# Kernel tuning notes

Hardware: AMD Instinct MI355X
Metric: run time of the kernel (lower is better)

## Reference

```python
import jax, jax.numpy as jnp
import numpy as np

N_NODES = 100000
N_EDGES = 1600000
N_GRAPHS = 64
VOCAB = 50000
D = 128
EPS = 1e-5


def setup_inputs() -> dict:
    key = jax.random.key(0)
    ks = jax.random.split(key, 24)
    tokens = jax.random.randint(ks[0], (N_NODES,), 0, VOCAB)
    src = jax.random.randint(ks[1], (N_EDGES,), 0, N_NODES)
    dst = jax.random.randint(ks[2], (N_EDGES,), 0, N_NODES)
    graph_ids = jnp.sort(jax.random.randint(ks[3], (N_NODES,), 0, N_GRAPHS))
    s = 1.0 / np.sqrt(D)
    inp = {
        'tokens': tokens, 'src': src, 'dst': dst, 'graph_ids': graph_ids,
        'embed': jax.random.normal(ks[4], (VOCAB, D), jnp.float32),
        'W1': jax.random.normal(ks[5], (D, D), jnp.float32) * s,
        'b1': jnp.zeros((D,), jnp.float32),
        'g1': jnp.ones((D,), jnp.float32), 'be1': jnp.zeros((D,), jnp.float32),
        'W2': jax.random.normal(ks[6], (D, D), jnp.float32) * s,
        'b2': jnp.zeros((D,), jnp.float32),
        'g2': jnp.ones((D,), jnp.float32), 'be2': jnp.zeros((D,), jnp.float32),
        'W3': jax.random.normal(ks[7], (D, D), jnp.float32) * s,
        'b3': jnp.zeros((D,), jnp.float32),
        'g3': jnp.ones((D,), jnp.float32), 'be3': jnp.zeros((D,), jnp.float32),
        'fcW1': jax.random.normal(ks[8], (D, D // 2), jnp.float32) * s,
        'fcb1': jnp.zeros((D // 2,), jnp.float32),
        'fcW2': jax.random.normal(ks[9], (D // 2, 2), jnp.float32) * (1.0 / np.sqrt(D // 2)),
        'fcb2': jnp.zeros((2,), jnp.float32),
    }
    return inp


def _graph_conv(h, src, dst, norm_src, norm_dst, W, b):
    # DGL GraphConv, norm='both': D_out^{-1/2} -> sum-aggregate -> D_in^{-1/2} -> linear
    msg = (h * norm_src[:, None])[src]                      # [E, D]
    agg = jax.ops.segment_sum(msg, dst, num_segments=N_NODES)
    return (agg * norm_dst[:, None]) @ W + b


def _bn_relu(h, gamma, beta):
    mu = jnp.mean(h, axis=0)
    var = jnp.mean((h - mu) ** 2, axis=0)                   # biased var (torch BN)
    return jax.nn.relu((h - mu) * jax.lax.rsqrt(var + EPS) * gamma + beta)


def reference(tokens, src, dst, graph_ids, embed,
              W1, b1, g1, be1, W2, b2, g2, be2, W3, b3, g3, be3,
              fcW1, fcb1, fcW2, fcb2):
    ones_e = jnp.ones((N_EDGES,), jnp.float32)
    deg_out = jnp.maximum(jax.ops.segment_sum(ones_e, src, num_segments=N_NODES), 1.0)
    deg_in = jnp.maximum(jax.ops.segment_sum(ones_e, dst, num_segments=N_NODES), 1.0)
    norm_src = jax.lax.rsqrt(deg_out)
    norm_dst = jax.lax.rsqrt(deg_in)

    h = embed[tokens]                                        # [N, D]
    h = _bn_relu(_graph_conv(h, src, dst, norm_src, norm_dst, W1, b1), g1, be1)
    h = _bn_relu(_graph_conv(h, src, dst, norm_src, norm_dst, W2, b2), g2, be2)
    h = _bn_relu(_graph_conv(h, src, dst, norm_src, norm_dst, W3, b3), g3, be3)

    # dgl.mean_nodes per graph
    sums = jax.ops.segment_sum(h, graph_ids, num_segments=N_GRAPHS)  # [G, D]
    cnts = jnp.maximum(jax.ops.segment_sum(jnp.ones((N_NODES,), jnp.float32), graph_ids, num_segments=N_GRAPHS), 1.0)
    hg = sums / cnts[:, None]

    hg = jax.nn.relu(hg @ fcW1 + fcb1)                       # dropout = identity (eval)
    return hg @ fcW2 + fcb2                                  # [G, 2]
```

## Files before the change

kernel.cpp:

```cpp
#include <hip/hip_runtime.h>

#define N_NODES 100000
#define N_EDGES 1600000
#define N_GRAPHS 64
#define DIM 128
#define BN_EPS 1e-5f
#define EPAD 2000000

#define NB_SENT 977
#define NB_WPREP 192
#define NB_HIST 391
#define NB_ZERO 40
#define NBUCK 782
#define NG (NBUCK * NB_HIST)
#define NB_SCANG2 2389
#define BUCK_RESERVE 388

#define AT_STRIDE 136

typedef unsigned short ushort_t;
typedef unsigned char uchar_t;
typedef unsigned int uint_t;
typedef __attribute__((ext_vector_type(8))) short bf16x8;
typedef __attribute__((ext_vector_type(4))) float f32x4;

__device__ __forceinline__ float bfl(uint_t u) {
    union { uint_t i; float f; } v; v.i = u << 16; return v.f;
}
__device__ __forceinline__ float bfh(uint_t u) {
    union { uint_t i; float f; } v; v.i = u & 0xffff0000u; return v.f;
}
__device__ __forceinline__ ushort_t f2bf(float f) {
    union { float f; uint_t i; } v; v.f = f;
    uint_t x = v.i;
    return (ushort_t)((x + 0x7fffu + ((x >> 16) & 1u)) >> 16);
}
__device__ __forceinline__ uint_t pack2(float lo, float hi) {
    return ((uint_t)f2bf(hi) << 16) | (uint_t)f2bf(lo);
}

__global__ void k_front(const int* __restrict__ src, const int* __restrict__ dst,
                        ushort_t* __restrict__ bufA, int* __restrict__ esrc,
                        const float* __restrict__ w1, const float* __restrict__ w2,
                        const float* __restrict__ w3, ushort_t* __restrict__ wbt,
                        int* __restrict__ GG, int* __restrict__ zp, int zwords) {
    __shared__ int hh[NBUCK];
    __shared__ int hh2[NBUCK];
    int b = blockIdx.x;
    int t = threadIdx.x;
    if (b < NB_SENT) {
        int i0 = (b * 256 + t) * 8;
        int4 sv = make_int4(N_NODES, N_NODES, N_NODES, N_NODES);
        if (i0 + 8 <= EPAD) {
            *(int4*)(esrc + i0) = sv;
            *(int4*)(esrc + i0 + 4) = sv;
        } else {
            for (int i = i0; i < EPAD; ++i) esrc[i] = N_NODES;
        }
        if (b == 0 && t < 64)
            ((uint_t*)(bufA + (size_t)N_NODES * DIM))[t] = 0u;
        return;
    }
    b -= NB_SENT;
    if (b < NB_WPREP) {
        int i = b * 256 + t;
        int l = i >> 14;
        int idx = i & (DIM * DIM - 1);
        int n = idx >> 7, k = idx & (DIM - 1);
        const float* wsrc = (l == 0) ? w1 : (l == 1) ? w2 : w3;
        wbt[i] = f2bf(wsrc[k * DIM + n]);
        return;
    }
    b -= NB_WPREP;
    if (b < NB_HIST) {
        for (int k = t; k < NBUCK; k += 256) { hh[k] = 0; hh2[k] = 0; }
        __syncthreads();
        int e0 = b * 4096;
        int e1 = min(e0 + 4096, N_EDGES);
        for (int i = e0 + t; i < e1; i += 256) {
            atomicAdd(&hh[dst[i] >> 7], 1);
            atomicAdd(&hh2[src[i] >> 7], 1);
        }
        __syncthreads();
        for (int k = t; k < NBUCK; k += 256) {
            GG[k * NB_HIST + b] = hh[k];
            GG[NG + k * NB_HIST + b] = hh2[k];
        }
        return;
    }
    b -= NB_HIST;
    {
        int i = b * 256 + t;
        if (i < zwords) zp[i] = 0;
    }
}

__global__ void k_scanA(const int* __restrict__ GG, int* __restrict__ Gs,
                        int* __restrict__ partials) {
    __shared__ int s[256];
    int t = threadIdx.x;
    int i = blockIdx.x * 256 + t;
    int v = (i < 2 * NG) ? GG[i] : 0;
    s[t] = v;
    __syncthreads();
    for (int off = 1; off < 256; off <<= 1) {
        int add = (t >= off) ? s[t - off] : 0;
        __syncthreads();
        s[t] += add;
        __syncthreads();
    }
    if (i < 2 * NG) Gs[i + 1] = s[t];
    if (t == 255) partials[blockIdx.x] = s[t];
}

__global__ void k_scanB(const int* __restrict__ partials, int* __restrict__ Gs) {
    __shared__ int s[256];
    int t = threadIdx.x;
    int p = 0;
    for (int j = t; j < (int)blockIdx.x; j += 256) p += partials[j];
    s[t] = p;
    __syncthreads();
    for (int off = 128; off > 0; off >>= 1) {
        if (t < off) s[t] += s[t + off];
        __syncthreads();
    }
    int prefix = s[0];
    int i = blockIdx.x * 256 + t;
    if (i < 2 * NG) Gs[i + 1] += prefix;
    if (blockIdx.x == 0 && t == 0) Gs[0] = 0;
}

__global__ void k_pass2(const int* __restrict__ src, const int* __restrict__ dst,
                        const int* __restrict__ Gs, uint_t* __restrict__ Cpk,
                        uchar_t* __restrict__ Cls) {
    __shared__ int cur[NBUCK];
    __shared__ int cur2[NBUCK];
    int b = blockIdx.x;
    int t = threadIdx.x;
    for (int k = t; k < NBUCK; k += 256) {
        cur[k] = Gs[k * NB_HIST + b];
        cur2[k] = Gs[NG + k * NB_HIST + b] - N_EDGES;
    }
    __syncthreads();
    int e0 = b * 4096;
    int e1 = min(e0 + 4096, N_EDGES);
    for (int i = e0 + t; i < e1; i += 256) {
        int d = dst[i];
        int s = src[i];
        int slot = atomicAdd(&cur[d >> 7], 1);
        Cpk[slot] = (uint_t)s | ((uint_t)(d & 127) << 17);
        int slot2 = atomicAdd(&cur2[s >> 7], 1);
        Cls[slot2] = (uchar_t)(s & 127);
    }
}

__global__ void k_fine(const uint_t* __restrict__ Cpk, const uchar_t* __restrict__ Cls,
                       const int* __restrict__ Gs,
                       const int* __restrict__ tokens, const float* __restrict__ embed,
                       int* __restrict__ esrc, int* __restrict__ rowptr,
                       int* __restrict__ pdeg, float* __restrict__ ns,
                       float* __restrict__ nd, ushort_t* __restrict__ bufA) {
    __shared__ int hcnt[128];
    __shared__ int hstart[128];
    __shared__ float lns[128];
    int b = blockIdx.x;
    int t = threadIdx.x;
    if (b < NBUCK) {
        int k = b;
        int node0 = k * 128;
        int nn = min(128, N_NODES - node0);
        int S = Gs[k * NB_HIST];
        int E = Gs[(k + 1) * NB_HIST];
        if (t < 128) hcnt[t] = 0;
        __syncthreads();
        for (int i = S + t; i < E; i += 256) atomicAdd(&hcnt[Cpk[i] >> 17], 1);
        __syncthreads();
        if (t == 0) {
            int acc = 0;
            for (int n = 0; n < nn; ++n) {
                hstart[n] = acc;
                acc += (hcnt[n] + 3) & ~3;
            }
        }
        __syncthreads();
        int base = (k * BUCK_RESERVE + S + 3) & ~3;
        if (t < nn) {
            int node = node0 + t;
            rowptr[node] = base + hstart[t];
            pdeg[node] = (hcnt[t] + 3) & ~3;
            nd[node] = rsqrtf(fmaxf((float)hcnt[t], 1.0f));
        }
        __syncthreads();
        for (int i = S + t; i < E; i += 256) {
            uint_t pk = Cpk[i];
            int slot = atomicAdd(&hstart[pk >> 17], 1);
            esrc[base + slot] = (int)(pk & 0x1FFFFu);
        }
    } else {
        int k = b - NBUCK;
        int node0 = k * 128;
        int nn = min(128, N_NODES - node0);
        int S = Gs[NG + k * NB_HIST] - N_EDGES;
        int E = Gs[NG + (k + 1) * NB_HIST] - N_EDGES;
        if (t < 128) hcnt[t] = 0;
        __syncthreads();
        for (int i = S + t; i < E; i += 256) atomicAdd(&hcnt[Cls[i]], 1);
        __syncthreads();
        if (t < nn) {
            float v = rsqrtf(fmaxf((float)hcnt[t], 1.0f));
            ns[node0 + t] = v;
            lns[t] = v;
        }
        if (k == 0 && t == 0) ns[N_NODES] = 0.f;
        __syncthreads();
        for (int slot = t; slot < nn * 16; slot += 256) {
            int nloc = slot >> 4, sub = slot & 15;
            int node = node0 + nloc;
            float s = lns[nloc];
            const float* ep = embed + (size_t)tokens[node] * DIM + sub * 8;
            float4 a = *(const float4*)ep;
            float4 c = *(const float4*)(ep + 4);
            uint4 o;
            o.x = pack2(a.x * s, a.y * s);
            o.y = pack2(a.z * s, a.w * s);
            o.z = pack2(c.x * s, c.y * s);
            o.w = pack2(c.z * s, c.w * s);
            *(uint4*)(bufA + (size_t)node * DIM + sub * 8) = o;
        }
    }
}

__global__ void k_prescale(const ushort_t* __restrict__ yin, const float* __restrict__ ns,
                           const float* __restrict__ bnsum, const float* __restrict__ bnsq,
                           const float* __restrict__ g, const float* __restrict__ be,
                           ushort_t* __restrict__ xout) {
    __shared__ float sa[DIM], sc[DIM];
    int t = threadIdx.x;
    if (t < DIM) {
        float mu = bnsum[t] * (1.0f / N_NODES);
        float var = bnsq[t] * (1.0f / N_NODES) - mu * mu;
        float rstd = rsqrtf(var + BN_EPS);
        float a = g[t] * rstd;
        sa[t] = a;
        sc[t] = be[t] - mu * a;
    }
    __syncthreads();
    int gid = blockIdx.x * 256 + t;
    int node = gid >> 4, sub = gid & 15;
    float s = ns[node];
    uint4 u = *(const uint4*)(yin + (size_t)node * DIM + sub * 8);
    float v[8] = {bfl(u.x), bfh(u.x), bfl(u.y), bfh(u.y),
                  bfl(u.z), bfh(u.z), bfl(u.w), bfh(u.w)};
    const float* a = sa + sub * 8;
    const float* c = sc + sub * 8;
#pragma unroll
    for (int i = 0; i < 8; ++i) v[i] = fmaxf(fmaf(v[i], a[i], c[i]), 0.f) * s;
    uint4 o;
    o.x = pack2(v[0], v[1]); o.y = pack2(v[2], v[3]);
    o.z = pack2(v[4], v[5]); o.w = pack2(v[6], v[7]);
    *(uint4*)(xout + (size_t)node * DIM + sub * 8) = o;
}

__global__ __launch_bounds__(256, 5) void k_agggemm(const ushort_t* __restrict__ hs,
        const int* __restrict__ rowptr, const int* __restrict__ pdeg,
        const int* __restrict__ esrc, const float* __restrict__ nd,
        const ushort_t* __restrict__ wbt, const float* __restrict__ bias,
        ushort_t* __restrict__ y,
        float* __restrict__ bnsum, float* __restrict__ bnsq) {
    __shared__ ushort_t at[64 * AT_STRIDE];
    __shared__ float csum[DIM], csq[DIM];
    int tid = threadIdx.x;
    int wave = tid >> 6;
    int lane = tid & 63;
    if (tid < DIM) { csum[tid] = 0.f; csq[tid] = 0.f; }
    __syncthreads();

    int bnode = blockIdx.x * 64 + wave * 16;
    int quad = lane >> 4;
    int m16 = lane & 15;

    const ushort_t* hrow = hs + (size_t)m16 * 8;

    int rpv = 0, pdv = 0;
    if (lane < 16) {
        int nnode = bnode + lane;
        if (nnode < N_NODES) { rpv = rowptr[nnode]; pdv = pdeg[nnode]; }
    }

#define FEATLD(ix) (*(const uint4*)(hrow + (size_t)(ix) * DIM))
#define ACCU(F, A)                                                  \
    {                                                               \
        A[0] += bfl((F).x); A[1] += bfh((F).x);                     \
        A[2] += bfl((F).y); A[3] += bfh((F).y);                     \
        A[4] += bfl((F).z); A[5] += bfh((F).z);                     \
        A[6] += bfl((F).w); A[7] += bfh((F).w);                     \
    }
#define DRAIN(E, T, A)                                              \
    {                                                               \
        if ((T) >= 2) {                                             \
            int i0_ = esrc[E], i1_ = esrc[(E) + 4];                 \
            (E) += 8; (T) -= 2;                                     \
            uint4 f0_ = FEATLD(i0_), f1_ = FEATLD(i1_);             \
            while ((T) >= 2) {                                      \
                int j0_ = esrc[E], j1_ = esrc[(E) + 4];             \
                (E) += 8; (T) -= 2;                                 \
                ACCU(f0_, A); ACCU(f1_, A);                         \
                f0_ = FEATLD(j0_); f1_ = FEATLD(j1_);               \
            }                                                       \
            ACCU(f0_, A); ACCU(f1_, A);                             \
        }                                                           \
        if (T) {                                                    \
            int i0_ = esrc[E];                                      \
            uint4 f0_ = FEATLD(i0_);                                \
            ACCU(f0_, A);                                           \
        }                                                           \
    }

    for (int i = 0; i < 16; i += 2) {
        int nodeA = bnode + i;
        int nodeB = bnode + i + 1;
        int eA = __shfl(rpv, i) + quad;
        int tA = __shfl(pdv, i) >> 2;
        int eB = __shfl(rpv, i + 1) + quad;
        int tB = __shfl(pdv, i + 1) >> 2;
        float aA[8] = {0.f, 0.f, 0.f, 0.f, 0.f, 0.f, 0.f, 0.f};
        float aB[8] = {0.f, 0.f, 0.f, 0.f, 0.f, 0.f, 0.f, 0.f};
        if (tA >= 2 && tB >= 2) {
            int iA0 = esrc[eA], iA1 = esrc[eA + 4];
            int iB0 = esrc[eB], iB1 = esrc[eB + 4];
            eA += 8; eB += 8; tA -= 2; tB -= 2;
            uint4 fA0 = FEATLD(iA0), fA1 = FEATLD(iA1);
            uint4 fB0 = FEATLD(iB0), fB1 = FEATLD(iB1);
            while (tA >= 2 && tB >= 2) {
                int jA0 = esrc[eA], jA1 = esrc[eA + 4];
                int jB0 = esrc[eB], jB1 = esrc[eB + 4];
                eA += 8; eB += 8; tA -= 2; tB -= 2;
                ACCU(fA0, aA); ACCU(fA1, aA);
                ACCU(fB0, aB); ACCU(fB1, aB);
                fA0 = FEATLD(jA0); fA1 = FEATLD(jA1);
                fB0 = FEATLD(jB0); fB1 = FEATLD(jB1);
            }
            ACCU(fA0, aA); ACCU(fA1, aA);
            ACCU(fB0, aB); ACCU(fB1, aB);
        }
        DRAIN(eA, tA, aA);
        DRAIN(eB, tB, aB);
#pragma unroll
        for (int j = 0; j < 8; ++j) {
            aA[j] += __shfl_xor(aA[j], 16);
            aA[j] += __shfl_xor(aA[j], 32);
            aB[j] += __shfl_xor(aB[j], 16);
            aB[j] += __shfl_xor(aB[j], 32);
        }
        float nA = (nodeA < N_NODES) ? nd[nodeA] : 0.f;
        float nB = (nodeB < N_NODES) ? nd[nodeB] : 0.f;
        if (quad == 0) {
            uint4 oA, oB;
            oA.x = pack2(aA[0] * nA, aA[1] * nA);
            oA.y = pack2(aA[2] * nA, aA[3] * nA);
            oA.z = pack2(aA[4] * nA, aA[5] * nA);
            oA.w = pack2(aA[6] * nA, aA[7] * nA);
            oB.x = pack2(aB[0] * nB, aB[1] * nB);
            oB.y = pack2(aB[2] * nB, aB[3] * nB);
            oB.z = pack2(aB[4] * nB, aB[5] * nB);
            oB.w = pack2(aB[6] * nB, aB[7] * nB);
            *(uint4*)&at[(wave * 16 + i) * AT_STRIDE + m16 * 8] = oA;
            *(uint4*)&at[(wave * 16 + i + 1) * AT_STRIDE + m16 * 8] = oB;
        }
    }
#undef DRAIN
#undef ACCU
#undef FEATLD

    f32x4 acc[8];
#pragma unroll
    for (int nb = 0; nb < 8; ++nb) acc[nb] = (f32x4)(0.f);

    const ushort_t* ap = &at[(wave * 16 + m16) * AT_STRIDE + quad * 8];
#pragma unroll
    for (int k0b = 0; k0b < 4; ++k0b) {
        bf16x8 af = *(const bf16x8*)(ap + k0b * 32);
#pragma unroll
        for (int nb = 0; nb < 8; ++nb) {
            int ncol = nb * 16 + m16;
            bf16x8 bfg = *(const bf16x8*)(wbt + (size_t)ncol * DIM + k0b * 32 + quad * 8);
            acc[nb] = __builtin_amdgcn_mfma_f32_16x16x32_bf16(af, bfg, acc[nb], 0, 0, 0);
        }
    }

#pragma unroll
    for (int nb = 0; nb < 8; ++nb) {
        int col = nb * 16 + m16;
        float bcol = bias[col];
        float ps = 0.f, pq = 0.f;
#pragma unroll
        for (int reg = 0; reg < 4; ++reg) {
            int r = bnode + quad * 4 + reg;
            if (r < N_NODES) {
                float v = acc[nb][reg] + bcol;
                ps += v; pq += v * v;
                y[(size_t)r * DIM + col] = f2bf(v);
            }
        }
        atomicAdd(&csum[col], ps);
        atomicAdd(&csq[col], pq);
    }
    __syncthreads();
    if (tid < DIM) {
        atomicAdd(&bnsum[tid], csum[tid]);
        atomicAdd(&bnsq[tid], csq[tid]);
    }
}

#define POOL_NODES 128
__global__ void k_pool(const ushort_t* __restrict__ yin, const int* __restrict__ gids,
                       const float* __restrict__ bnsum, const float* __restrict__ bnsq,
                       const float* __restrict__ g, const float* __restrict__ be,
                       float* __restrict__ pool, int* __restrict__ cnt) {
    __shared__ int h[N_GRAPHS];
    int col = threadIdx.x;
    float mu = bnsum[col] * (1.0f / N_NODES);
    float var = bnsq[col] * (1.0f / N_NODES) - mu * mu;
    float rstd = rsqrtf(var + BN_EPS);
    float a = g[col] * rstd;
    float c = be[col] - mu * a;
    if (col < N_GRAPHS) h[col] = 0;
    __syncthreads();
    int base = blockIdx.x * POOL_NODES;
    int end = min(base + POOL_NODES, N_NODES);
    for (int n = base + col; n < end; n += 128) atomicAdd(&h[gids[n]], 1);
    __syncthreads();
    if (col < N_GRAPHS && h[col]) atomicAdd(&cnt[col], h[col]);
    float acc = 0.f;
    int cur = gids[base];
    for (int n = base; n < end; ++n) {
        int gg = gids[n];
        if (gg != cur) {
            atomicAdd(&pool[(size_t)cur * DIM + col], acc);
            acc = 0.f;
            cur = gg;
        }
        uint_t u = *(const uint_t*)(yin + (size_t)n * DIM + (col & ~1));
        float v = (col & 1) ? bfh(u) : bfl(u);
        acc += fmaxf(fmaf(v, a, c), 0.f);
    }
    atomicAdd(&pool[(size_t)cur * DIM + col], acc);
}

__global__ void k_final(const float* __restrict__ pool, const int* __restrict__ cnt,
                        const float* __restrict__ fcW1, const float* __restrict__ fcb1,
                        const float* __restrict__ fcW2, const float* __restrict__ fcb2,
                        float* __restrict__ out) {
    __shared__ float hg[DIM];
    __shared__ float z[64];
    int g = blockIdx.x;
    int t = threadIdx.x;
    float cf = fmaxf((float)cnt[g], 1.0f);
    hg[t] = pool[(size_t)g * DIM + t] / cf;
    __syncthreads();
    if (t < 64) {
        float acc = fcb1[t];
        for (int k = 0; k < DIM; ++k)
            acc += hg[k] * fcW1[k * 64 + t];
        z[t] = fmaxf(acc, 0.f);
    }
    __syncthreads();
    if (t < 2) {
        float acc = fcb2[t];
        for (int k = 0; k < 64; ++k)
            acc += z[k] * fcW2[k * 2 + t];
        out[g * 2 + t] = acc;
    }
}

extern "C" void kernel_launch(void* const* d_in, const int* in_sizes, int n_in,
                              void* d_out, int out_size, void* d_ws, size_t ws_size,
                              hipStream_t stream) {
    const int* tokens = (const int*)d_in[0];
    const int* src = (const int*)d_in[1];
    const int* dst = (const int*)d_in[2];
    const int* gids = (const int*)d_in[3];
    const float* embed = (const float*)d_in[4];
    const float* W1 = (const float*)d_in[5];
    const float* b1 = (const float*)d_in[6];
    const float* g1 = (const float*)d_in[7];
    const float* be1 = (const float*)d_in[8];
    const float* W2 = (const float*)d_in[9];
    const float* b2 = (const float*)d_in[10];
    const float* g2 = (const float*)d_in[11];
    const float* be2 = (const float*)d_in[12];
    const float* W3 = (const float*)d_in[13];
    const float* b3 = (const float*)d_in[14];
    const float* g3 = (const float*)d_in[15];
    const float* be3 = (const float*)d_in[16];
    const float* fcW1 = (const float*)d_in[17];
    const float* fcb1 = (const float*)d_in[18];
    const float* fcW2 = (const float*)d_in[19];
    const float* fcb2 = (const float*)d_in[20];
    float* out = (float*)d_out;

    char* w = (char*)d_ws;
    auto alloc = [&](size_t bytes) {
        void* p = (void*)w;
        w += (bytes + 255) & ~(size_t)255;
        return p;
    };
    ushort_t* bufH = (ushort_t*)alloc((size_t)(N_NODES + 1) * DIM * 2);
    ushort_t* bufA = (ushort_t*)alloc((size_t)(N_NODES + 1) * DIM * 2);
    ushort_t* bufY = (ushort_t*)alloc((size_t)(N_NODES + 1) * DIM * 2);
    int* esrc = (int*)alloc((size_t)EPAD * 4);
    int* rowptr = (int*)alloc((size_t)N_NODES * 4);
    int* pdeg = (int*)alloc((size_t)N_NODES * 4);
    float* ns = (float*)alloc((size_t)(N_NODES + 1) * 4);
    float* nd = (float*)alloc((size_t)N_NODES * 4);
    ushort_t* wbt = (ushort_t*)alloc(3 * DIM * DIM * 2);
    int* GG = (int*)alloc((size_t)(2 * NG) * 4);
    int* Gs = (int*)alloc((size_t)(2 * NG + 1) * 4);
    int* partials = (int*)alloc(4096 * 4);
    uint_t* Cpk = (uint_t*)alloc((size_t)N_EDGES * 4);
    uchar_t* Cls = (uchar_t*)alloc((size_t)N_EDGES);
    char* zstart = w;
    float* bnsum = (float*)alloc(3 * DIM * 4);
    float* bnsq = (float*)alloc(3 * DIM * 4);
    float* pool = (float*)alloc((size_t)N_GRAPHS * DIM * 4);
    int* cnt = (int*)alloc((size_t)N_GRAPHS * 4);
    int zwords = (int)((size_t)(w - zstart) / 4);

    k_front<<<NB_SENT + NB_WPREP + NB_HIST + NB_ZERO, 256, 0, stream>>>(
        src, dst, bufA, esrc, W1, W2, W3, wbt, GG, (int*)zstart, zwords);
    k_scanA<<<NB_SCANG2, 256, 0, stream>>>(GG, Gs, partials);
    k_scanB<<<NB_SCANG2, 256, 0, stream>>>(partials, Gs);
    k_pass2<<<NB_HIST, 256, 0, stream>>>(src, dst, Gs, Cpk, Cls);
    k_fine<<<2 * NBUCK, 256, 0, stream>>>(Cpk, Cls, Gs, tokens, embed,
                                          esrc, rowptr, pdeg, ns, nd, bufA);

    int nb_fused = (N_NODES + 63) / 64;
    int nb_ps = 6250;

    k_agggemm<<<nb_fused, 256, 0, stream>>>(bufA, rowptr, pdeg, esrc, nd,
                                            wbt, b1, bufY, bnsum, bnsq);
    k_prescale<<<nb_ps, 256, 0, stream>>>(bufY, ns, bnsum, bnsq, g1, be1, bufA);
    k_agggemm<<<nb_fused, 256, 0, stream>>>(bufA, rowptr, pdeg, esrc, nd,
                                            wbt + (size_t)DIM * DIM, b2, bufH,
                                            bnsum + DIM, bnsq + DIM);
    k_prescale<<<nb_ps, 256, 0, stream>>>(bufH, ns, bnsum + DIM, bnsq + DIM, g2, be2, bufA);
    k_agggemm<<<nb_fused, 256, 0, stream>>>(bufA, rowptr, pdeg, esrc, nd,
                                            wbt + (size_t)2 * DIM * DIM, b3, bufY,
                                            bnsum + 2 * DIM, bnsq + 2 * DIM);

    k_pool<<<(N_NODES + POOL_NODES - 1) / POOL_NODES, DIM, 0, stream>>>(
        bufY, gids, bnsum + 2 * DIM, bnsq + 2 * DIM, g3, be3, pool, cnt);
    k_final<<<N_GRAPHS, DIM, 0, stream>>>(pool, cnt, fcW1, fcb1, fcW2, fcb2, out);
}
```

Measured before the change: 667.0 us.

## Stream a wave's edges as one continuous pipelined loop across its 16 nodes

The per-node-pair gather loop is replaced by a single flat loop over the wave's whole contiguous edge range. It keeps four feature loads in flight and flushes the accumulator to LDS at each node boundary. This removes the per-node pipeline ramp-up and drain and the imbalance between paired nodes of different degree, so memory latency is hidden better for low-degree nodes. The occupancy hint in launch_bounds is dropped, which frees more registers for the deeper prefetch but may lower the number of waves per CU. The code also relies on padded edges, prefetching past the end of the range into the padded buffer.

```diff
diff --git a/kernel.cpp b/kernel.cpp
--- a/kernel.cpp
+++ b/kernel.cpp
@@ -261,7 +261,7 @@
     *(uint4*)(xout + (size_t)node * DIM + sub * 8) = o;
 }
 
-__global__ __launch_bounds__(256, 5) void k_agggemm(const ushort_t* __restrict__ hs,
+__global__ __launch_bounds__(256) void k_agggemm(const ushort_t* __restrict__ hs,
         const int* __restrict__ rowptr, const int* __restrict__ pdeg,
         const int* __restrict__ esrc, const float* __restrict__ nd,
         const ushort_t* __restrict__ wbt, const float* __restrict__ bias,
@@ -281,94 +281,77 @@
 
     const ushort_t* hrow = hs + (size_t)m16 * 8;
 
-    int rpv = 0, pdv = 0;
+    int rpv = 0, epv = 0;
+    float ndv = 0.f;
     if (lane < 16) {
         int nnode = bnode + lane;
-        if (nnode < N_NODES) { rpv = rowptr[nnode]; pdv = pdeg[nnode]; }
-    }
+        if (nnode < N_NODES) {
+            rpv = rowptr[nnode];
+            epv = rpv + pdeg[nnode];
+            ndv = nd[nnode];
+        }
+    }
+    int ws = __shfl(rpv, 0);
+    int T = (__shfl(epv, 15) - ws) >> 2;
 
 #define FEATLD(ix) (*(const uint4*)(hrow + (size_t)(ix) * DIM))
-#define ACCU(F, A)                                                  \
+#define ACCU(F)                                                     \
     {                                                               \
-        A[0] += bfl((F).x); A[1] += bfh((F).x);                     \
-        A[2] += bfl((F).y); A[3] += bfh((F).y);                     \
-        A[4] += bfl((F).z); A[5] += bfh((F).z);                     \
-        A[6] += bfl((F).w); A[7] += bfh((F).w);                     \
-    }
-#define DRAIN(E, T, A)                                              \
+        a[0] += bfl((F).x); a[1] += bfh((F).x);                     \
+        a[2] += bfl((F).y); a[3] += bfh((F).y);                     \
+        a[4] += bfl((F).z); a[5] += bfh((F).z);                     \
+        a[6] += bfl((F).w); a[7] += bfh((F).w);                     \
+    }
+#define FLUSH()                                                     \
     {                                                               \
-        if ((T) >= 2) {                                             \
-            int i0_ = esrc[E], i1_ = esrc[(E) + 4];                 \
-            (E) += 8; (T) -= 2;                                     \
-            uint4 f0_ = FEATLD(i0_), f1_ = FEATLD(i1_);             \
-            while ((T) >= 2) {                                      \
-                int j0_ = esrc[E], j1_ = esrc[(E) + 4];             \
-                (E) += 8; (T) -= 2;                                 \
-                ACCU(f0_, A); ACCU(f1_, A);                         \
-                f0_ = FEATLD(j0_); f1_ = FEATLD(j1_);               \
-            }                                                       \
-            ACCU(f0_, A); ACCU(f1_, A);                             \
+        float nv = __shfl(ndv, ni);                                 \
+        _Pragma("unroll")                                           \
+        for (int j = 0; j < 8; ++j) {                               \
+            a[j] += __shfl_xor(a[j], 16);                           \
+            a[j] += __shfl_xor(a[j], 32);                           \
         }                                                           \
-        if (T) {                                                    \
-            int i0_ = esrc[E];                                      \
-            uint4 f0_ = FEATLD(i0_);                                \
-            ACCU(f0_, A);                                           \
+        if (quad == 0) {                                            \
+            uint4 o;                                                \
+            o.x = pack2(a[0] * nv, a[1] * nv);                      \
+            o.y = pack2(a[2] * nv, a[3] * nv);                      \
+            o.z = pack2(a[4] * nv, a[5] * nv);                      \
+            o.w = pack2(a[6] * nv, a[7] * nv);                      \
+            *(uint4*)&at[(wave * 16 + ni) * AT_STRIDE + m16 * 8] = o; \
         }                                                           \
-    }
-
-    for (int i = 0; i < 16; i += 2) {
-        int nodeA = bnode + i;
-        int nodeB = bnode + i + 1;
-        int eA = __shfl(rpv, i) + quad;
-        int tA = __shfl(pdv, i) >> 2;
-        int eB = __shfl(rpv, i + 1) + quad;
-        int tB = __shfl(pdv, i + 1) >> 2;
-        float aA[8] = {0.f, 0.f, 0.f, 0.f, 0.f, 0.f, 0.f, 0.f};
-        float aB[8] = {0.f, 0.f, 0.f, 0.f, 0.f, 0.f, 0.f, 0.f};
-        if (tA >= 2 && tB >= 2) {
-            int iA0 = esrc[eA], iA1 = esrc[eA + 4];
-            int iB0 = esrc[eB], iB1 = esrc[eB + 4];
-            eA += 8; eB += 8; tA -= 2; tB -= 2;
-            uint4 fA0 = FEATLD(iA0), fA1 = FEATLD(iA1);
-            uint4 fB0 = FEATLD(iB0), fB1 = FEATLD(iB1);
-            while (tA >= 2 && tB >= 2) {
-                int jA0 = esrc[eA], jA1 = esrc[eA + 4];
-                int jB0 = esrc[eB], jB1 = esrc[eB + 4];
-                eA += 8; eB += 8; tA -= 2; tB -= 2;
-                ACCU(fA0, aA); ACCU(fA1, aA);
-                ACCU(fB0, aB); ACCU(fB1, aB);
-                fA0 = FEATLD(jA0); fA1 = FEATLD(jA1);
-                fB0 = FEATLD(jB0); fB1 = FEATLD(jB1);
-            }
-            ACCU(fA0, aA); ACCU(fA1, aA);
-            ACCU(fB0, aB); ACCU(fB1, aB);
-        }
-        DRAIN(eA, tA, aA);
-        DRAIN(eB, tB, aB);
-#pragma unroll
-        for (int j = 0; j < 8; ++j) {
-            aA[j] += __shfl_xor(aA[j], 16);
-            aA[j] += __shfl_xor(aA[j], 32);
-            aB[j] += __shfl_xor(aB[j], 16);
-            aB[j] += __shfl_xor(aB[j], 32);
-        }
-        float nA = (nodeA < N_NODES) ? nd[nodeA] : 0.f;
-        float nB = (nodeB < N_NODES) ? nd[nodeB] : 0.f;
-        if (quad == 0) {
-            uint4 oA, oB;
-            oA.x = pack2(aA[0] * nA, aA[1] * nA);
-            oA.y = pack2(aA[2] * nA, aA[3] * nA);
-            oA.z = pack2(aA[4] * nA, aA[5] * nA);
-            oA.w = pack2(aA[6] * nA, aA[7] * nA);
-            oB.x = pack2(aB[0] * nB, aB[1] * nB);
-            oB.y = pack2(aB[2] * nB, aB[3] * nB);
-            oB.z = pack2(aB[4] * nB, aB[5] * nB);
-            oB.w = pack2(aB[6] * nB, aB[7] * nB);
-            *(uint4*)&at[(wave * 16 + i) * AT_STRIDE + m16 * 8] = oA;
-            *(uint4*)&at[(wave * 16 + i + 1) * AT_STRIDE + m16 * 8] = oB;
-        }
-    }
-#undef DRAIN
+        _Pragma("unroll")                                           \
+        for (int j = 0; j < 8; ++j) a[j] = 0.f;                     \
+    }
+#define BCHK()                                                      \
+    while (ni < 16 && pos >= end_cur) {                             \
+        FLUSH();                                                    \
+        ++ni;                                                       \
+        end_cur = __shfl(epv, ni < 16 ? ni : 15);                   \
+    }
+
+    float a[8] = {0.f, 0.f, 0.f, 0.f, 0.f, 0.f, 0.f, 0.f};
+    int ni = 0;
+    int end_cur = __shfl(epv, 0);
+    int pos = ws + 4;
+
+    int sl = ws + quad;
+    int i0 = esrc[sl], i1 = esrc[sl + 4], i2 = esrc[sl + 8], i3 = esrc[sl + 12];
+    uint4 f0 = FEATLD(i0), f1 = FEATLD(i1), f2 = FEATLD(i2), f3 = FEATLD(i3);
+    i0 = esrc[sl + 16]; i1 = esrc[sl + 20]; i2 = esrc[sl + 24]; i3 = esrc[sl + 28];
+    sl += 32;
+
+    int t = 0;
+    for (; t + 4 <= T; t += 4) {
+        { int n_ = esrc[sl]; sl += 4; ACCU(f0); f0 = FEATLD(i0); i0 = n_; BCHK(); pos += 4; }
+        { int n_ = esrc[sl]; sl += 4; ACCU(f1); f1 = FEATLD(i1); i1 = n_; BCHK(); pos += 4; }
+        { int n_ = esrc[sl]; sl += 4; ACCU(f2); f2 = FEATLD(i2); i2 = n_; BCHK(); pos += 4; }
+        { int n_ = esrc[sl]; sl += 4; ACCU(f3); f3 = FEATLD(i3); i3 = n_; BCHK(); pos += 4; }
+    }
+    if (t + 0 < T) { ACCU(f0); BCHK(); pos += 4; }
+    if (t + 1 < T) { ACCU(f1); BCHK(); pos += 4; }
+    if (t + 2 < T) { ACCU(f2); BCHK(); pos += 4; }
+    while (ni < 16) { FLUSH(); ++ni; }
+#undef BCHK
+#undef FLUSH
 #undef ACCU
 #undef FEATLD
 
```

New measurement: 604.0 us. -9.4%, faster.
